# Optimization experiments

Measured on AMD Instinct MI355X. Metric: run time of the kernel, lower is better.

The kernel has to match this reference:

```python
import jax, jax.numpy as jnp
import numpy as np

N = 40000
IN_DIM = 2000
HID = 512
OUT_DIM = 30
E = 400000


def setup_inputs() -> dict:
    key = jax.random.key(0)
    k1, k2, k3, k4, k5, k6 = jax.random.split(key, 6)
    features = jax.random.normal(k1, (N, IN_DIM), dtype=jnp.float32)
    edge_index = jax.random.randint(k2, (2, E), 0, N, dtype=jnp.int64)
    # xavier_normal_(gain=1.414): std = gain * sqrt(2/(fan_in+fan_out))
    W1 = jax.random.normal(k3, (IN_DIM, HID), dtype=jnp.float32) * (1.414 * np.sqrt(2.0 / (IN_DIM + HID)))
    W2 = jax.random.normal(k4, (HID, OUT_DIM), dtype=jnp.float32) * (1.414 * np.sqrt(2.0 / (HID + OUT_DIM)))
    att_src = jax.random.normal(k5, (HID,), dtype=jnp.float32) * (1.414 * np.sqrt(2.0 / (1 + HID)))
    att_dst = jax.random.normal(k6, (HID,), dtype=jnp.float32) * (1.414 * np.sqrt(2.0 / (1 + HID)))
    return {"features": features, "W1": W1, "W2": W2,
            "att_src": att_src, "att_dst": att_dst, "edge_index": edge_index}


def _gat_propagate(x_proj, alpha_src, alpha_dst, src, dst, n_nodes):
    """GATConv message+aggregate (heads=1, aggr='add').
    x_proj: [N, C] projected features; alpha_src/alpha_dst: [N] per-node scores.
    """
    score = jax.nn.sigmoid(alpha_src[src] + alpha_dst[dst])          # [E]
    # segment softmax over destination neighborhoods (PyG softmax)
    seg_max = jax.ops.segment_max(score, dst, num_segments=n_nodes)  # [N]
    e = jnp.exp(score - seg_max[dst])                                # [E]
    seg_sum = jax.ops.segment_sum(e, dst, num_segments=n_nodes)     # [N]
    alpha = e / (seg_sum[dst] + 1e-16)                               # [E]
    msg = x_proj[src] * alpha[:, None]                               # [E, C] gather + scale
    return jax.ops.segment_sum(msg, dst, num_segments=n_nodes)      # [N, C] scatter-add


def _stagate_forward(features, W1, W2, att_src, att_dst, src, dst):
    n = features.shape[0]
    # conv1: attention=True (computes its own alpha)
    x1 = features @ W1                                # [N, HID]
    a_src = x1 @ att_src                              # [N]
    a_dst = x1 @ att_dst                              # [N]
    h1 = jax.nn.elu(_gat_propagate(x1, a_src, a_dst, src, dst, n))
    # conv2: attention=False -> just linear projection (heads=1 mean)
    h2 = h1 @ W2                                      # [N, OUT_DIM]
    # conv3: weights tied to W2^T, attention tied to conv1's alphas
    x3 = h2 @ W2.T                                    # [N, HID]
    h3 = jax.nn.elu(_gat_propagate(x3, a_src, a_dst, src, dst, n))
    # conv4: attention=False, weights tied to W1^T
    h4 = h3 @ W1.T                                    # [N, IN_DIM]
    return h2, h4


def reference(features, W1, W2, att_src, att_dst, edge_index):
    src = edge_index[0]
    dst = edge_index[1]
    return _stagate_forward(features, W1, W2, att_src, att_dst, src, dst)
```

## Files before the change

### kernel.cpp

```cpp
#include <hip/hip_runtime.h>
#include <cstdint>

#define NNODES 40000
#define INDIM 2000
#define HIDD 512
#define ODIM 30
#define NEDGES 400000
#define KPAD 2048
#define ROWSPLIT 20224

typedef short bf16x8 __attribute__((ext_vector_type(8)));
typedef float f32x4 __attribute__((ext_vector_type(4)));

__device__ __forceinline__ float bf2f(ushort u){ union{unsigned int i; float f;} x; x.i = ((unsigned int)u)<<16; return x.f; }
__device__ __forceinline__ ushort f2bf(float v){ union{float f; unsigned int u;} x; x.f=v; unsigned int r = x.u + 0x7fffu + ((x.u>>16)&1u); return (ushort)(r>>16); }

__device__ __forceinline__ int xcd_swz(int orig, int nwg){
  int q = nwg >> 3, r = nwg & 7;
  int xcd = orig & 7;
  int idx = orig >> 3;
  return (xcd < r ? xcd*(q+1) : r*(q+1) + (xcd-r)*q) + idx;
}

#define P_MID  asm volatile("" ::: "memory"); __builtin_amdgcn_s_barrier(); \
               asm volatile("s_waitcnt lgkmcnt(0)" ::: "memory"); \
               __builtin_amdgcn_sched_barrier(0); __builtin_amdgcn_s_setprio(1);
#define P_END  __builtin_amdgcn_s_setprio(0); asm volatile("" ::: "memory"); \
               __builtin_amdgcn_s_barrier(); __builtin_amdgcn_sched_barrier(0);
#define P_ENDW __builtin_amdgcn_s_setprio(0); \
               asm volatile("s_waitcnt vmcnt(4)" ::: "memory"); \
               asm volatile("" ::: "memory"); __builtin_amdgcn_s_barrier(); \
               __builtin_amdgcn_sched_barrier(0);

template<typename OutT>
__device__ __forceinline__ void gemm_body(
    const ushort* __restrict__ A, const ushort* __restrict__ Bt,
    OutT* __restrict__ C, int M, int N, int K, int ldc,
    int row0, int col0, char* smem)
{
  ushort* Al = (ushort*)smem;
  ushort* Bl = (ushort*)(smem + 65536);
  const int tid = threadIdx.x;
  const int lane = tid & 63;
  const int w = tid >> 6;
  const int wm = w >> 2, wn = w & 3;
  const int NT = K >> 6;

  f32x4 acc[8][4] = {};
  bf16x8 a[4][2], b[4][2];

  auto stage = [&](bool isA, int kt, int h){
    const ushort* G = isA ? A : Bt;
    int base = isA ? row0 : col0;
    int lim  = isA ? M : N;
    ushort* L = (isA ? Al : Bl) + ((kt & 1) << 14);
    if (kt >= NT) kt -= NT;
    #pragma unroll
    for (int it = 0; it < 2; ++it){
      int ch = tid + (it << 9);
      int rl = (h << 7) + (ch >> 3);
      int cs = ch & 7;
      int gr = base + rl; gr = gr < lim ? gr : lim - 1;
      int gc = (kt << 6) + ((cs ^ (rl & 7)) << 3);
      __builtin_amdgcn_global_load_lds(
        (const __attribute__((address_space(1))) unsigned int*)(G + (size_t)gr*K + gc),
        (__attribute__((address_space(3))) unsigned int*)(L + rl*64 + cs*8), 16, 0, 0);
    }
  };
  auto lda = [&](int buf, int mf, int kk) -> bf16x8 {
    int rl = wm*128 + mf*16 + (lane & 15);
    int ko = kk*32 + ((lane >> 4) << 3);
    return *(const bf16x8*)&Al[(buf << 14) + rl*64 + (ko ^ ((rl & 7) << 3))];
  };
  auto ldb = [&](int buf, int nf, int kk) -> bf16x8 {
    int rl = wn*64 + nf*16 + (lane & 15);
    int ko = kk*32 + ((lane >> 4) << 3);
    return *(const bf16x8*)&Bl[(buf << 14) + rl*64 + (ko ^ ((rl & 7) << 3))];
  };
  auto mfma_q = [&](int mbase, int nbase){
    #pragma unroll
    for (int i=0;i<4;++i)
      #pragma unroll
      for (int j=0;j<2;++j)
        #pragma unroll
        for (int kk=0;kk<2;++kk)
          acc[mbase+i][nbase+j] = __builtin_amdgcn_mfma_f32_16x16x32_bf16(
              a[i][kk], b[nbase+j][kk], acc[mbase+i][nbase+j], 0, 0, 0);
  };

  stage(false, 0, 0); stage(false, 0, 1);
  stage(true , 0, 0); stage(true , 0, 1);
  stage(false, 1, 0); stage(false, 1, 1);
  asm volatile("s_waitcnt vmcnt(4)" ::: "memory");
  asm volatile("" ::: "memory");
  __builtin_amdgcn_s_barrier();
  __builtin_amdgcn_sched_barrier(0);

  const int NT2 = NT >> 1;
  for (int t = 0; t < NT2; ++t){
    const int kt0 = 2*t, kt1 = 2*t + 1;
    #pragma unroll
    for (int i=0;i<4;++i){ a[i][0]=lda(0,i,0); a[i][1]=lda(0,i,1); }
    #pragma unroll
    for (int j=0;j<2;++j){ b[j][0]=ldb(0,j,0); b[j][1]=ldb(0,j,1); }
    stage(true, kt1, 0);
    P_MID; mfma_q(0,0); P_END;
    #pragma unroll
    for (int j=2;j<4;++j){ b[j][0]=ldb(0,j,0); b[j][1]=ldb(0,j,1); }
    stage(true, kt1, 1);
    P_MID; mfma_q(0,2); P_END;
    #pragma unroll
    for (int i=0;i<4;++i){ a[i][0]=lda(0,4+i,0); a[i][1]=lda(0,4+i,1); }
    stage(false, kt0+2, 0);
    P_MID; mfma_q(4,0); P_END;
    stage(false, kt0+2, 1);
    P_MID; mfma_q(4,2); P_ENDW;
    #pragma unroll
    for (int i=0;i<4;++i){ a[i][0]=lda(1,i,0); a[i][1]=lda(1,i,1); }
    #pragma unroll
    for (int j=0;j<2;++j){ b[j][0]=ldb(1,j,0); b[j][1]=ldb(1,j,1); }
    stage(true, kt0+2, 0);
    P_MID; mfma_q(0,0); P_END;
    #pragma unroll
    for (int j=2;j<4;++j){ b[j][0]=ldb(1,j,0); b[j][1]=ldb(1,j,1); }
    stage(true, kt0+2, 1);
    P_MID; mfma_q(0,2); P_END;
    #pragma unroll
    for (int i=0;i<4;++i){ a[i][0]=lda(1,4+i,0); a[i][1]=lda(1,4+i,1); }
    stage(false, kt1+2, 0);
    P_MID; mfma_q(4,0); P_END;
    stage(false, kt1+2, 1);
    P_MID; mfma_q(4,2); P_ENDW;
  }

  asm volatile("s_waitcnt vmcnt(0)" ::: "memory");
  __syncthreads();

  if constexpr (sizeof(OutT)==2) {
    ushort* cs = (ushort*)smem;
    #pragma unroll
    for (int p=0;p<2;++p){
      if (wm == p){
        #pragma unroll
        for (int mf=0;mf<8;++mf)
          #pragma unroll
          for (int nf=0;nf<4;++nf)
            #pragma unroll
            for (int reg=0;reg<4;++reg)
              cs[(mf*16 + ((lane>>4)<<2) + reg)*264 + wn*64 + nf*16 + (lane&15)] = f2bf(acc[mf][nf][reg]);
      }
      __syncthreads();
      #pragma unroll
      for (int it=0; it<8; ++it){
        int ch = tid + it*512;
        int r = ch >> 5, c8 = (ch & 31) * 8;
        int gr = row0 + p*128 + r;
        if (gr < M && col0 + c8 + 8 <= N)
          *(bf16x8*)&((ushort*)C)[(size_t)gr*ldc + col0 + c8] = *(const bf16x8*)&cs[r*264 + c8];
      }
      __syncthreads();
    }
  } else {
    float* cf = (float*)smem;
    #pragma unroll
    for (int p=0;p<4;++p){
      if (wm == (p>>1)){
        int mh = (p & 1) * 4;
        #pragma unroll
        for (int i=0;i<4;++i)
          #pragma unroll
          for (int nf=0;nf<4;++nf)
            #pragma unroll
            for (int reg=0;reg<4;++reg)
              cf[(i*16 + ((lane>>4)<<2) + reg)*260 + wn*64 + nf*16 + (lane&15)] = acc[mh+i][nf][reg];
      }
      __syncthreads();
      #pragma unroll
      for (int it=0; it<8; ++it){
        int ch = tid + it*512;
        int r = ch >> 6, c4 = (ch & 63) * 4;
        int gr = row0 + p*64 + r, gc = col0 + c4;
        if (gr < M && gc + 4 <= N)
          *(f32x4*)&((float*)C)[(size_t)gr*ldc + gc] = *(const f32x4*)&cf[r*260 + c4];
      }
      __syncthreads();
    }
  }
}

__device__ __forceinline__ void cast_rows2(const float* __restrict__ features,
    ushort* __restrict__ featb, int row_base, int cb){
  int t = threadIdx.x;
  int row = row_base + (cb<<1) + (t>>8);
  int kc = t & 255;
  bf16x8 o;
  if (kc < INDIM/8) {
    const float* p = features + (size_t)row*INDIM + kc*8;
    #pragma unroll
    for (int j=0;j<8;++j) o[j] = (short)f2bf(p[j]);
  } else {
    #pragma unroll
    for (int j=0;j<8;++j) o[j] = 0;
  }
  *(bf16x8*)(featb + (size_t)row*KPAD + kc*8) = o;
}

__device__ __forceinline__ void scan_body(const int* __restrict__ degp,
    int* __restrict__ row_ptr, int* part){
  const int t = threadIdx.x;
  const int base = t * 80;
  int s = 0;
  for (int j=0;j<80;++j){ int i = base+j; s += (i < NNODES) ? degp[i] : 0; }
  part[t] = s;
  __syncthreads();
  for (int off=1; off<512; off<<=1){
    int x = (t >= off) ? part[t-off] : 0;
    __syncthreads();
    part[t] += x;
    __syncthreads();
  }
  int run = (t > 0) ? part[t-1] : 0;
  for (int j=0;j<80;++j){
    int i = base+j;
    if (i <= NNODES){
      row_ptr[i] = run;
      if (i < NNODES) run += degp[i];
    }
  }
}

#define S1_CAST   10112
#define S1_W1     (S1_CAST + 2000)
#define S1_W2     (S1_W1 + 32)
#define S1_HIST   (S1_W2 + 782)
#define S1_PAD    (S1_HIST + 48)
#define S1_CUR    (S1_PAD + 79)

__global__ __launch_bounds__(512) void setup_kernel(
    const float* __restrict__ features, const float* __restrict__ W1, const float* __restrict__ W2,
    const int* __restrict__ edst,
    ushort* __restrict__ featb, ushort* __restrict__ W1b, ushort* __restrict__ W1t,
    ushort* __restrict__ W2p, ushort* __restrict__ W2tc,
    int* __restrict__ deg, int* __restrict__ cursor){
  int b = blockIdx.x, t = threadIdx.x;
  if (b < S1_CAST){
    cast_rows2(features, featb, 0, b);
  } else if (b < S1_W1){
    int idx = (b - S1_CAST)*512 + t;
    int r = idx >> 9, c = idx & 511;
    ushort bb = f2bf(W1[idx]);
    W1b[idx] = bb;
    W1t[(size_t)c*KPAD + r] = bb;
  } else if (b < S1_W2){
    int idx = (b - S1_W1)*512 + t;
    int k = idx >> 5, c = idx & 31;
    float val = (c < ODIM) ? W2[k*ODIM + c] : 0.f;
    ushort bb = f2bf(val);
    W2p[k*32 + c] = bb;
    W2tc[c*HIDD + k] = bb;
  } else if (b < S1_HIST){
    int e = (b - S1_W2)*512 + t;
    if (e < NEDGES) atomicAdd(&deg[edst[e]], 1);
  } else if (b < S1_PAD){
    int z = (b - S1_HIST)*512 + t;
    int c = z / 48, r = 2000 + (z - c*48);
    W1t[(size_t)c*KPAD + r] = 0;
  } else {
    int z = (b - S1_PAD)*512 + t;
    if (z < NNODES) cursor[z] = 0;
  }
}

#define K2_G 158
__global__ __launch_bounds__(512, 2) void gemm1a_kernel(
    const ushort* __restrict__ featb, const ushort* __restrict__ W1t, ushort* __restrict__ x1,
    const float* __restrict__ features, ushort* __restrict__ featb_w,
    const int* __restrict__ deg, int* __restrict__ row_ptr){
  __shared__ __align__(16) char smem[131072];
  int b = blockIdx.x;
  if (b < K2_G){
    int s = xcd_swz(b, K2_G);
    int row0 = (s >> 1) << 8;
    int col0 = (s & 1) << 8;
    gemm_body<ushort>(featb, W1t, x1, NNODES, HIDD, KPAD, HIDD, row0, col0, smem);
  } else if (b == K2_G){
    scan_body(deg, row_ptr, (int*)smem);
  } else {
    cast_rows2(features, featb_w, ROWSPLIT, b - K2_G - 1);
  }
}

#define K3_G 156
#define K3_PL (K3_G + 782)
__global__ __launch_bounds__(512, 2) void gemm1b_kernel(
    const ushort* __restrict__ featb, const ushort* __restrict__ W1t, ushort* __restrict__ x1,
    const int* __restrict__ esrc, const int* __restrict__ edst,
    const int* __restrict__ row_ptr, int* __restrict__ cursor, int* __restrict__ csr_src,
    const float* __restrict__ att_src, const float* __restrict__ att_dst,
    float* __restrict__ a_src, float* __restrict__ a_dst){
  __shared__ __align__(16) char smem[131072];
  int b = blockIdx.x, t = threadIdx.x;
  if (b < K3_G){
    int s = xcd_swz(b, K3_G);
    int row0 = ROWSPLIT + ((s >> 1) << 8);
    int col0 = (s & 1) << 8;
    gemm_body<ushort>(featb, W1t, x1, NNODES, HIDD, KPAD, HIDD, row0, col0, smem);
  } else if (b < K3_PL){
    int e = (b - K3_G)*512 + t;
    if (e < NEDGES){
      int d = edst[e];
      int pos = row_ptr[d] + atomicAdd(&cursor[d], 1);
      csr_src[pos] = esrc[e];
    }
  } else {
    int gid = (b - K3_PL)*512 + t;
    int row = gid >> 6, lane = gid & 63;
    bf16x8 v = *(const bf16x8*)(x1 + (size_t)row*HIDD + lane*8);
    float ps = 0.f, pd = 0.f;
    #pragma unroll
    for (int j=0;j<8;++j){
      float xv = bf2f((ushort)v[j]);
      ps += xv * att_src[lane*8+j];
      pd += xv * att_dst[lane*8+j];
    }
    #pragma unroll
    for (int off=32; off>0; off>>=1){ ps += __shfl_down(ps, off); pd += __shfl_down(pd, off); }
    if (lane == 0){ a_src[row] = ps; a_dst[row] = pd; }
  }
}

__global__ __launch_bounds__(512) void a2_kernel(const ushort* __restrict__ x1,
    const float* __restrict__ att_src, const float* __restrict__ att_dst,
    float* __restrict__ a_src, float* __restrict__ a_dst){
  int gid = blockIdx.x*512 + threadIdx.x;
  int row = ROWSPLIT + (gid >> 6), lane = gid & 63;
  if (row >= NNODES) return;
  bf16x8 v = *(const bf16x8*)(x1 + (size_t)row*HIDD + lane*8);
  float ps = 0.f, pd = 0.f;
  #pragma unroll
  for (int j=0;j<8;++j){
    float xv = bf2f((ushort)v[j]);
    ps += xv * att_src[lane*8+j];
    pd += xv * att_dst[lane*8+j];
  }
  #pragma unroll
  for (int off=32; off>0; off>>=1){ ps += __shfl_down(ps, off); pd += __shfl_down(pd, off); }
  if (lane == 0){ a_src[row] = ps; a_dst[row] = pd; }
}

__global__ __launch_bounds__(256) void alpha_kernel(const int* __restrict__ row_ptr,
    const int* __restrict__ csr_src, const float* __restrict__ a_src,
    const float* __restrict__ a_dst, float* __restrict__ csr_alpha){
  int gid = blockIdx.x*256 + threadIdx.x;
  int v = gid >> 4, lane = gid & 15;
  if (v >= NNODES) return;
  int p0 = row_ptr[v], p1 = row_ptr[v+1];
  if (p0 >= p1) return;
  float ad = a_dst[v];
  float m = -1e30f;
  for (int p = p0 + lane; p < p1; p += 16){
    float s = 1.f/(1.f + __expf(-(a_src[csr_src[p]] + ad)));
    m = fmaxf(m, s);
  }
  #pragma unroll
  for (int off=8; off>0; off>>=1) m = fmaxf(m, __shfl_xor(m, off));
  float sum = 0.f;
  for (int p = p0 + lane; p < p1; p += 16){
    float s = 1.f/(1.f + __expf(-(a_src[csr_src[p]] + ad)));
    float e = __expf(s - m);
    csr_alpha[p] = e;
    sum += e;
  }
  #pragma unroll
  for (int off=8; off>0; off>>=1) sum += __shfl_xor(sum, off);
  float inv = 1.f/(sum + 1e-16f);
  for (int p = p0 + lane; p < p1; p += 16) csr_alpha[p] *= inv;
}

__global__ __launch_bounds__(256) void agg1_kernel(const ushort* __restrict__ X,
    const int* __restrict__ row_ptr, const int* __restrict__ csr_src,
    const float* __restrict__ csr_alpha, ushort* __restrict__ outb){
  int gid = blockIdx.x*256 + threadIdx.x;
  int v = gid >> 6, lane = gid & 63;
  if (v >= NNODES) return;
  int p0 = __builtin_amdgcn_readfirstlane(row_ptr[v]);
  int p1 = __builtin_amdgcn_readfirstlane(row_ptr[v+1]);
  float acc[8] = {0.f,0.f,0.f,0.f,0.f,0.f,0.f,0.f};
  int p = p0;
  for (; p + 8 <= p1; p += 8){
    int s[8]; float A[8];
    #pragma unroll
    for (int u=0;u<8;++u){ s[u] = csr_src[p+u]; A[u] = csr_alpha[p+u]; }
    bf16x8 x[8];
    #pragma unroll
    for (int u=0;u<8;++u) x[u] = *(const bf16x8*)(X + (size_t)s[u]*HIDD + lane*8);
    #pragma unroll
    for (int u=0;u<8;++u)
      #pragma unroll
      for (int k=0;k<8;++k) acc[k] += A[u] * bf2f((ushort)x[u][k]);
  }
  for (; p + 4 <= p1; p += 4){
    int s0 = csr_src[p], s1 = csr_src[p+1], s2 = csr_src[p+2], s3 = csr_src[p+3];
    float A0 = csr_alpha[p], A1 = csr_alpha[p+1], A2 = csr_alpha[p+2], A3 = csr_alpha[p+3];
    bf16x8 x0 = *(const bf16x8*)(X + (size_t)s0*HIDD + lane*8);
    bf16x8 x1 = *(const bf16x8*)(X + (size_t)s1*HIDD + lane*8);
    bf16x8 x2 = *(const bf16x8*)(X + (size_t)s2*HIDD + lane*8);
    bf16x8 x3 = *(const bf16x8*)(X + (size_t)s3*HIDD + lane*8);
    #pragma unroll
    for (int k=0;k<8;++k)
      acc[k] += A0*bf2f((ushort)x0[k]) + A1*bf2f((ushort)x1[k])
              + A2*bf2f((ushort)x2[k]) + A3*bf2f((ushort)x3[k]);
  }
  for (; p < p1; ++p){
    int sj = csr_src[p];
    float aj = csr_alpha[p];
    bf16x8 xv = *(const bf16x8*)(X + (size_t)sj*HIDD + lane*8);
    #pragma unroll
    for (int k=0;k<8;++k) acc[k] += aj * bf2f((ushort)xv[k]);
  }
  bf16x8 o;
  #pragma unroll
  for (int k=0;k<8;++k){
    float a = acc[k];
    a = a > 0.f ? a : __expf(a)-1.f;
    o[k] = (short)f2bf(a);
  }
  *(bf16x8*)(outb + (size_t)v*HIDD + lane*8) = o;
}

__global__ __launch_bounds__(256) void mid_kernel(const ushort* __restrict__ h1,
    const ushort* __restrict__ W2tc, float* __restrict__ h2){
  __shared__ ushort h1s[32*512];
  __shared__ ushort w2s[32*512];
  const int t = threadIdx.x;
  const int row0 = blockIdx.x * 32;
  const ushort* g = h1 + (size_t)row0*HIDD;
  #pragma unroll
  for (int it=0; it<8; ++it){
    int ch = t + it*256;
    *(bf16x8*)&h1s[ch*8] = *(const bf16x8*)&g[ch*8];
    *(bf16x8*)&w2s[ch*8] = *(const bf16x8*)&W2tc[ch*8];
  }
  __syncthreads();
  int c = t & 31, rg = t >> 5;
  if (c < ODIM){
    float acc[4] = {0.f,0.f,0.f,0.f};
    for (int k0=0;k0<64;++k0){
      bf16x8 wv = *(const bf16x8*)&w2s[c*512 + k0*8];
      #pragma unroll
      for (int rr=0; rr<4; ++rr){
        bf16x8 hv = *(const bf16x8*)&h1s[(rg*4+rr)*HIDD + k0*8];
        #pragma unroll
        for (int j=0;j<8;++j) acc[rr] += bf2f((ushort)hv[j]) * bf2f((ushort)wv[j]);
      }
    }
    #pragma unroll
    for (int rr=0;rr<4;++rr) h2[(size_t)(row0 + rg*4 + rr)*ODIM + c] = acc[rr];
  }
}

__global__ __launch_bounds__(256) void conv3_kernel(const float* __restrict__ h2,
    const int* __restrict__ row_ptr, const int* __restrict__ csr_src,
    const float* __restrict__ csr_alpha, const ushort* __restrict__ W2p,
    ushort* __restrict__ h3){
  int gid = blockIdx.x*256 + threadIdx.x;
  int v = gid >> 6, lane = gid & 63;
  if (v >= NNODES) return;
  int p0 = __builtin_amdgcn_readfirstlane(row_ptr[v]);
  int p1 = __builtin_amdgcn_readfirstlane(row_ptr[v+1]);
  float accd = 0.f;
  if (lane < ODIM){
    int p = p0;
    for (; p + 4 <= p1; p += 4){
      int s0 = csr_src[p], s1 = csr_src[p+1], s2 = csr_src[p+2], s3 = csr_src[p+3];
      float a0 = csr_alpha[p], a1 = csr_alpha[p+1], a2 = csr_alpha[p+2], a3 = csr_alpha[p+3];
      accd += a0*h2[(size_t)s0*ODIM + lane] + a1*h2[(size_t)s1*ODIM + lane]
            + a2*h2[(size_t)s2*ODIM + lane] + a3*h2[(size_t)s3*ODIM + lane];
    }
    for (; p < p1; ++p)
      accd += csr_alpha[p] * h2[(size_t)csr_src[p]*ODIM + lane];
  }
  float gv[ODIM];
  #pragma unroll
  for (int ci=0; ci<ODIM; ++ci) gv[ci] = __shfl(accd, ci);
  #pragma unroll
  for (int it=0; it<8; ++it){
    int n = it*64 + lane;
    const ushort* wrp = W2p + n*32;
    bf16x8 wvv[4];
    #pragma unroll
    for (int qd=0;qd<4;++qd) wvv[qd] = *(const bf16x8*)(wrp + qd*8);
    float acc = 0.f;
    #pragma unroll
    for (int ci=0; ci<ODIM; ++ci) acc += gv[ci]*bf2f((ushort)wvv[ci>>3][ci&7]);
    acc = acc > 0.f ? acc : __expf(acc)-1.f;
    h3[(size_t)v*HIDD + n] = f2bf(acc);
  }
}

template<typename OutT>
__global__ __launch_bounds__(512, 2) void gemm8_kernel(
    const ushort* __restrict__ A, const ushort* __restrict__ Bt,
    OutT* __restrict__ C, int M, int N, int K, int ldc, int nwg, int cshift)
{
  __shared__ __align__(16) char smem[131072];
  int s = xcd_swz(blockIdx.x, nwg);
  int row0 = (s >> cshift) << 8;
  int col0 = (s & ((1 << cshift) - 1)) << 8;
  gemm_body<OutT>(A, Bt, C, M, N, K, ldc, row0, col0, smem);
}

extern "C" void kernel_launch(void* const* d_in, const int* in_sizes, int n_in,
                              void* d_out, int out_size, void* d_ws, size_t ws_size,
                              hipStream_t stream){
  const float* features = (const float*)d_in[0];
  const float* W1 = (const float*)d_in[1];
  const float* W2 = (const float*)d_in[2];
  const float* att_src = (const float*)d_in[3];
  const float* att_dst = (const float*)d_in[4];
  const int* edge = (const int*)d_in[5];
  const int* esrc = edge;
  const int* edst = edge + NEDGES;

  float* h2 = (float*)d_out;
  float* h4 = h2 + (size_t)NNODES*ODIM;
  char* obase = (char*)h4;
  ushort* featb = (ushort*)obase;
  ushort* x1b   = (ushort*)(obase + 163840000);
  ushort* h1b   = (ushort*)(obase + 204800000);

  char* wbase = (char*)d_ws;
  size_t o = 0;
  auto walloc = [&](size_t bytes)->void*{ void* p = wbase + o; o += (bytes + 255) & ~(size_t)255; return p; };
  ushort* h3b      = (ushort*)walloc((size_t)NNODES*HIDD*2);
  ushort* W1b      = (ushort*)walloc((size_t)INDIM*HIDD*2);
  ushort* W1t      = (ushort*)walloc((size_t)HIDD*KPAD*2);
  ushort* W2p      = (ushort*)walloc(512*32*2);
  ushort* W2tc     = (ushort*)walloc(32*512*2);
  float*  a_src    = (float*)walloc(NNODES*4);
  float*  a_dst    = (float*)walloc(NNODES*4);
  int*    deg      = (int*)walloc(NNODES*4);
  int*    cursor   = (int*)walloc(NNODES*4);
  int*    row_ptr  = (int*)walloc((NNODES+1)*4);
  int*    csr_src  = (int*)walloc(NEDGES*4);
  float*  csr_alpha= (float*)walloc(NEDGES*4);

  hipMemsetAsync(deg, 0, NNODES*4, stream);

  setup_kernel<<<S1_CUR, 512, 0, stream>>>(features, W1, W2, edst,
      featb, W1b, W1t, W2p, W2tc, deg, cursor);

  gemm1a_kernel<<<K2_G + 1 + 9888, 512, 0, stream>>>(featb, W1t, x1b,
      features, featb, deg, row_ptr);

  gemm1b_kernel<<<K3_PL + 2528, 512, 0, stream>>>(featb, W1t, x1b,
      esrc, edst, row_ptr, cursor, csr_src, att_src, att_dst, a_src, a_dst);

  a2_kernel<<<2472, 512, 0, stream>>>(x1b, att_src, att_dst, a_src, a_dst);

  alpha_kernel<<<2500, 256, 0, stream>>>(row_ptr, csr_src, a_src, a_dst, csr_alpha);

  agg1_kernel<<<10000, 256, 0, stream>>>(x1b, row_ptr, csr_src, csr_alpha, h1b);
  mid_kernel<<<NNODES/32, 256, 0, stream>>>(h1b, W2tc, h2);
  conv3_kernel<<<10000, 256, 0, stream>>>(h2, row_ptr, csr_src, csr_alpha, W2p, h3b);
  gemm8_kernel<float><<<1256, 512, 0, stream>>>(h3b, W1b, h4,
      NNODES, INDIM, HIDD, INDIM, 1256, 3);
}
```

Measured before the change: 593.4 us.

## Fuse conv3 aggregation into final GEMM with per-panel spin barrier

Merges the conv3 gather/project kernel and the final h3@W1^T GEMM into one launch. Each block computes 32 rows of h3, then waits on a per-panel atomic counter until all 8 blocks producing its 256-row panel finish, and then runs its GEMM tile. This is meant to remove the kernel boundary and let panels start the GEMM early. It relies on co-residency and in-order block dispatch for forward progress, and it drops the XCD swizzle on tile mapping.

```diff
diff --git a/kernel.cpp b/kernel.cpp
--- a/kernel.cpp
+++ b/kernel.cpp
@@ -229,6 +229,42 @@
   }
 }
 
+__device__ __forceinline__ void conv3_node(int v, int lane,
+    const float* __restrict__ h2, const int* __restrict__ row_ptr,
+    const int* __restrict__ csr_src, const float* __restrict__ csr_alpha,
+    const ushort* __restrict__ W2p, ushort* __restrict__ h3){
+  int p0 = __builtin_amdgcn_readfirstlane(row_ptr[v]);
+  int p1 = __builtin_amdgcn_readfirstlane(row_ptr[v+1]);
+  float accd = 0.f;
+  if (lane < ODIM){
+    int p = p0;
+    for (; p + 4 <= p1; p += 4){
+      int s0 = csr_src[p], s1 = csr_src[p+1], s2 = csr_src[p+2], s3 = csr_src[p+3];
+      float a0 = csr_alpha[p], a1 = csr_alpha[p+1], a2 = csr_alpha[p+2], a3 = csr_alpha[p+3];
+      accd += a0*h2[(size_t)s0*ODIM + lane] + a1*h2[(size_t)s1*ODIM + lane]
+            + a2*h2[(size_t)s2*ODIM + lane] + a3*h2[(size_t)s3*ODIM + lane];
+    }
+    for (; p < p1; ++p)
+      accd += csr_alpha[p] * h2[(size_t)csr_src[p]*ODIM + lane];
+  }
+  float gv[ODIM];
+  #pragma unroll
+  for (int ci=0; ci<ODIM; ++ci) gv[ci] = __shfl(accd, ci);
+  #pragma unroll
+  for (int it=0; it<8; ++it){
+    int n = it*64 + lane;
+    const ushort* wrp = W2p + n*32;
+    bf16x8 wvv[4];
+    #pragma unroll
+    for (int qd=0;qd<4;++qd) wvv[qd] = *(const bf16x8*)(wrp + qd*8);
+    float acc = 0.f;
+    #pragma unroll
+    for (int ci=0; ci<ODIM; ++ci) acc += gv[ci]*bf2f((ushort)wvv[ci>>3][ci&7]);
+    acc = acc > 0.f ? acc : __expf(acc)-1.f;
+    h3[(size_t)v*HIDD + n] = f2bf(acc);
+  }
+}
+
 #define S1_CAST   10112
 #define S1_W1     (S1_CAST + 2000)
 #define S1_W2     (S1_W1 + 32)
@@ -241,7 +277,7 @@
     const int* __restrict__ edst,
     ushort* __restrict__ featb, ushort* __restrict__ W1b, ushort* __restrict__ W1t,
     ushort* __restrict__ W2p, ushort* __restrict__ W2tc,
-    int* __restrict__ deg, int* __restrict__ cursor){
+    int* __restrict__ deg, int* __restrict__ cursor, int* __restrict__ panel_cnt){
   int b = blockIdx.x, t = threadIdx.x;
   if (b < S1_CAST){
     cast_rows2(features, featb, 0, b);
@@ -268,6 +304,7 @@
   } else {
     int z = (b - S1_PAD)*512 + t;
     if (z < NNODES) cursor[z] = 0;
+    else if (z < NNODES + 157) panel_cnt[z - NNODES] = 0;
   }
 }
 
@@ -459,55 +496,31 @@
   }
 }
 
-__global__ __launch_bounds__(256) void conv3_kernel(const float* __restrict__ h2,
-    const int* __restrict__ row_ptr, const int* __restrict__ csr_src,
-    const float* __restrict__ csr_alpha, const ushort* __restrict__ W2p,
-    ushort* __restrict__ h3){
-  int gid = blockIdx.x*256 + threadIdx.x;
-  int v = gid >> 6, lane = gid & 63;
-  if (v >= NNODES) return;
-  int p0 = __builtin_amdgcn_readfirstlane(row_ptr[v]);
-  int p1 = __builtin_amdgcn_readfirstlane(row_ptr[v+1]);
-  float accd = 0.f;
-  if (lane < ODIM){
-    int p = p0;
-    for (; p + 4 <= p1; p += 4){
-      int s0 = csr_src[p], s1 = csr_src[p+1], s2 = csr_src[p+2], s3 = csr_src[p+3];
-      float a0 = csr_alpha[p], a1 = csr_alpha[p+1], a2 = csr_alpha[p+2], a3 = csr_alpha[p+3];
-      accd += a0*h2[(size_t)s0*ODIM + lane] + a1*h2[(size_t)s1*ODIM + lane]
-            + a2*h2[(size_t)s2*ODIM + lane] + a3*h2[(size_t)s3*ODIM + lane];
-    }
-    for (; p < p1; ++p)
-      accd += csr_alpha[p] * h2[(size_t)csr_src[p]*ODIM + lane];
-  }
-  float gv[ODIM];
-  #pragma unroll
-  for (int ci=0; ci<ODIM; ++ci) gv[ci] = __shfl(accd, ci);
-  #pragma unroll
-  for (int it=0; it<8; ++it){
-    int n = it*64 + lane;
-    const ushort* wrp = W2p + n*32;
-    bf16x8 wvv[4];
-    #pragma unroll
-    for (int qd=0;qd<4;++qd) wvv[qd] = *(const bf16x8*)(wrp + qd*8);
-    float acc = 0.f;
-    #pragma unroll
-    for (int ci=0; ci<ODIM; ++ci) acc += gv[ci]*bf2f((ushort)wvv[ci>>3][ci&7]);
-    acc = acc > 0.f ? acc : __expf(acc)-1.f;
-    h3[(size_t)v*HIDD + n] = f2bf(acc);
-  }
-}
-
-template<typename OutT>
-__global__ __launch_bounds__(512, 2) void gemm8_kernel(
-    const ushort* __restrict__ A, const ushort* __restrict__ Bt,
-    OutT* __restrict__ C, int M, int N, int K, int ldc, int nwg, int cshift)
-{
+__global__ __launch_bounds__(512, 2) void conv3_gemm4_kernel(
+    const float* __restrict__ h2, const int* __restrict__ row_ptr,
+    const int* __restrict__ csr_src, const float* __restrict__ csr_alpha,
+    const ushort* __restrict__ W2p, ushort* __restrict__ h3,
+    const ushort* __restrict__ W1b, float* __restrict__ h4,
+    int* __restrict__ panel_cnt){
   __shared__ __align__(16) char smem[131072];
-  int s = xcd_swz(blockIdx.x, nwg);
-  int row0 = (s >> cshift) << 8;
-  int col0 = (s & ((1 << cshift) - 1)) << 8;
-  gemm_body<OutT>(A, Bt, C, M, N, K, ldc, row0, col0, smem);
+  const int g = blockIdx.x, tid = threadIdx.x;
+  const int lane = tid & 63, wv = tid >> 6;
+  #pragma unroll
+  for (int i=0;i<4;++i){
+    int v = 32*g + wv*4 + i;
+    if (v < NNODES) conv3_node(v, lane, h2, row_ptr, csr_src, csr_alpha, W2p, h3);
+  }
+  __threadfence();
+  __syncthreads();
+  if (tid == 0){
+    atomicAdd(&panel_cnt[g >> 3], 1);
+    while (atomicAdd(&panel_cnt[g >> 3], 0) < 8) __builtin_amdgcn_s_sleep(2);
+  }
+  __syncthreads();
+  __threadfence();
+  int row0 = (g >> 3) << 8;
+  int col0 = (g & 7) << 8;
+  gemm_body<float>(h3, W1b, h4, NNODES, INDIM, HIDD, INDIM, row0, col0, smem);
 }
 
 extern "C" void kernel_launch(void* const* d_in, const int* in_sizes, int n_in,
@@ -544,11 +557,12 @@
   int*    row_ptr  = (int*)walloc((NNODES+1)*4);
   int*    csr_src  = (int*)walloc(NEDGES*4);
   float*  csr_alpha= (float*)walloc(NEDGES*4);
+  int*    panel_cnt= (int*)walloc(157*4);
 
   hipMemsetAsync(deg, 0, NNODES*4, stream);
 
   setup_kernel<<<S1_CUR, 512, 0, stream>>>(features, W1, W2, edst,
-      featb, W1b, W1t, W2p, W2tc, deg, cursor);
+      featb, W1b, W1t, W2p, W2tc, deg, cursor, panel_cnt);
 
   gemm1a_kernel<<<K2_G + 1 + 9888, 512, 0, stream>>>(featb, W1t, x1b,
       features, featb, deg, row_ptr);
@@ -562,7 +576,7 @@
 
   agg1_kernel<<<10000, 256, 0, stream>>>(x1b, row_ptr, csr_src, csr_alpha, h1b);
   mid_kernel<<<NNODES/32, 256, 0, stream>>>(h1b, W2tc, h2);
-  conv3_kernel<<<10000, 256, 0, stream>>>(h2, row_ptr, csr_src, csr_alpha, W2p, h3b);
-  gemm8_kernel<float><<<1256, 512, 0, stream>>>(h3b, W1b, h4,
-      NNODES, INDIM, HIDD, INDIM, 1256, 3);
-}
+
+  conv3_gemm4_kernel<<<1256, 512, 0, stream>>>(h2, row_ptr, csr_src, csr_alpha,
+      W2p, h3b, W1b, h4, panel_cnt);
+}
```

Result: slower. 1.095 ms (+84.6%).
